# Kernel tuning notes

Measured on AMD Instinct MI355X. Metric: run time of the kernel, lower is better.

Reference implementation:

```python
import jax, jax.numpy as jnp
import numpy as np

BLOCK = 4  # block_size from init_kwargs


def space_to_channel_3d(x, b):
    # Faithful translation of SpaceToChannel_3d.forward (torch split/stack/permute chain).
    B, C, W, H, D = x.shape
    y = x.transpose(0, 2, 3, 4, 1)                      # (B, W, H, D, C)
    y = y.reshape(B, W, H, D // b, b, C)                # split depth into D//b chunks of b
    y = y.transpose(0, 3, 1, 2, 4, 5)                   # (B, D//b, W, H, b, C)
    y = y.reshape(B, D // b, W // b, H // b, C * b * b * b)  # per-chunk row-major reshape
    y = y.transpose(0, 2, 3, 1, 4)                      # (B, W//b, H//b, D//b, C*b^3)
    return y.transpose(0, 4, 1, 2, 3)                   # (B, C*b^3, W//b, H//b, D//b)


def channel_to_space_3d(x, b):
    # Faithful translation of ChannelToSpace_3d.forward.
    B, Cd, wd, hd, dd = x.shape
    b3 = b * b * b
    Cs = Cd // b3
    y = x.transpose(0, 2, 3, 4, 1)                      # (B, wd, hd, dd, Cd)
    y = y.reshape(B, wd, hd, dd, b * b, b, Cs)          # split b^3 dim into b^2 chunks of b
    y = y.transpose(0, 4, 1, 2, 3, 5, 6)                # (B, b^2, wd, hd, dd, b, Cs)
    y = y.reshape(B, b * b, wd, hd, dd * b, Cs)         # merge (dd, b) per chunk
    y = y.transpose(0, 2, 1, 3, 4, 5)                   # (B, wd, b^2, hd, dd*b, Cs)
    y = y.reshape(B, wd * b, hd * b, dd * b, Cs)        # row-major merge of (wd, b^2, hd)
    return y.transpose(0, 4, 1, 2, 3)                   # (B, Cs, wd*b, hd*b, dd*b)


def setup_inputs() -> dict:
    key = jax.random.key(0)
    k1, k2 = jax.random.split(key)
    x = jax.random.normal(k1, (4, 32, 64, 64, 64), dtype=jnp.float32)
    gamma = jax.random.normal(k2, (1,), dtype=jnp.float32)
    return {"x": x, "gamma": gamma}


def reference(x, gamma):
    b = BLOCK
    y = space_to_channel_3d(x, b)                       # (B, C*b^3, w, h, d)
    B, C, w, h, d = y.shape
    q = y.reshape(B, C, w * h * d)                      # (B, C', N)
    # channel-wise attention: energy (B, C', C')
    energy = jnp.einsum('bcn,ben->bce', q, q)
    energy_new = jnp.max(energy, axis=-1, keepdims=True) - energy
    attention = jax.nn.softmax(energy_new, axis=-1)
    out = jnp.einsum('bce,ben->bcn', attention, q)      # (B, C', N)
    out = out.reshape(B, C, w, h, d)
    out = gamma * out + y
    return channel_to_space_3d(out, b)
```

## Files before the change

### kernel.cpp

```cpp
#include <hip/hip_runtime.h>

typedef _Float16 f16;
typedef __attribute__((ext_vector_type(8))) _Float16 f16x8;
typedef __attribute__((ext_vector_type(4))) float f32x4;

#define CCH 2048
#define NSP 4096
#define NB  4

__device__ __forceinline__ void gld16(const void* g, void* l) {
  __builtin_amdgcn_global_load_lds(
      (const __attribute__((address_space(1))) void*)g,
      (__attribute__((address_space(3))) void*)l, 16, 0, 0);
}

__global__ void pack_kernel(const float* __restrict__ x, f16* __restrict__ qh,
                            f16* __restrict__ ql, int b0) {
  int gid = blockIdx.x * 256 + threadIdx.x;
  int n = gid & (NSP - 1);
  int t = gid >> 12;
  int c = t & 31; t >>= 5;
  int r = t & 15; int ib = t >> 4;
  int wc = n >> 8, hc = (n >> 4) & 15, dc = n & 15;
  int w = wc * 4 + (hc >> 2);
  int h = (hc & 3) * 16 + r;
  int b = b0 + ib;
  const f32x4 v = *(const f32x4*)(x + ((((size_t)b * 32 + c) * 64 + w) * 64 + h) * 64 + dc * 4);
#pragma unroll
  for (int bd = 0; bd < 4; ++bd) {
    int cc = r * 128 + bd * 32 + c;
    size_t o = ((size_t)ib * CCH + cc) * NSP + n;
    float val = v[bd];
    f16 hi = (f16)val;
    qh[o] = hi;
    ql[o] = (f16)(val - (float)hi);
  }
}

__global__ void transpose_kernel(const f16* __restrict__ qh, f16* __restrict__ qhT) {
  int ib = blockIdx.z;
  int j0 = blockIdx.x * 64, n0 = blockIdx.y * 64;
  __shared__ f16 tile[64][72];
  int t = threadIdx.x;
  int r = t >> 3;
  int cb = (t & 7) * 8;
#pragma unroll
  for (int half = 0; half < 2; ++half) {
    int rr = r + half * 32;
    f16x8 v = *(const f16x8*)(qh + ((size_t)ib * CCH + j0 + rr) * NSP + n0 + cb);
    *(f16x8*)&tile[rr][cb] = v;
  }
  __syncthreads();
#pragma unroll
  for (int half = 0; half < 2; ++half) {
    int rr = r + half * 32;
    f16x8 o;
#pragma unroll
    for (int u = 0; u < 8; ++u) o[u] = tile[cb + u][rr];
    *(f16x8*)(qhT + ((size_t)ib * NSP + n0 + rr) * CCH + j0 + cb) = o;
  }
}

__global__ __launch_bounds__(256) void gemm1_kernel(const f16* __restrict__ qh,
                                                    const f16* __restrict__ ql,
                                                    float* __restrict__ energy,
                                                    int ksplit) {
  int ib = blockIdx.z;
  int nwg = gridDim.x;
  int cpx = nwg >> 3;
  int bx = blockIdx.x;
  int tri = (bx & 7) * cpx + (bx >> 3);
  int ks = 0;
  if (ksplit == 2) { ks = tri >= 136; tri -= ks * 136; }
  int rem = tri, bi = 0, span = 16;
  while (rem >= span) { rem -= span; ++bi; --span; }
  int bj = bi + rem;
  int i0 = bi * 128, j0 = bj * 128;
  int kbeg = ks * 2048;
  int kend = (ksplit == 2) ? kbeg + 2048 : NSP;
  float* eout = energy + ((size_t)(ks * gridDim.z + ib)) * CCH * CCH;

  __shared__ f16 Lds[2][4][128 * 32];
  int tid = threadIdx.x;
  int lane = tid & 63, wv = tid >> 6;
  int l15 = lane & 15, quad = lane >> 4;
  int wr = (wv >> 1) * 64, wcol = (wv & 1) * 64;
  int swz = (l15 >> 1) & 3;
  int kbs = (lane & 3) ^ ((lane >> 3) & 3);

  const f16* srcA = (wv & 1) ? ql : qh;
  int rbase = (wv < 2) ? i0 : j0;
  const f16* gsrc = srcA + ((size_t)ib * CCH + rbase) * NSP
                    + (size_t)(lane >> 2) * NSP + kbs * 8;

  auto stage = [&](int buf, int kk) {
    f16* ld = &Lds[buf][wv][0];
#pragma unroll
    for (int t = 0; t < 8; ++t)
      gld16(gsrc + (size_t)(t * 16) * NSP + kk, ld + t * 512);
  };

  const f32x4 vzero = {0.f, 0.f, 0.f, 0.f};
  f32x4 acc[4][4];
#pragma unroll
  for (int a = 0; a < 4; ++a)
#pragma unroll
    for (int bq = 0; bq < 4; ++bq) acc[a][bq] = vzero;

  int nk = (kend - kbeg) >> 5;
  stage(0, kbeg);
  __syncthreads();
  for (int it = 0; it < nk; ++it) {
    int cur = it & 1;
    if (it + 1 < nk) stage(cur ^ 1, kbeg + ((it + 1) << 5));
    f16x8 ah[4], al[4], bh[4], bl[4];
#pragma unroll
    for (int mt = 0; mt < 4; ++mt) {
      int row = wr + mt * 16 + l15;
      ah[mt] = *(const f16x8*)&Lds[cur][0][row * 32 + ((quad ^ swz) * 8)];
      al[mt] = *(const f16x8*)&Lds[cur][1][row * 32 + ((quad ^ swz) * 8)];
    }
#pragma unroll
    for (int nt = 0; nt < 4; ++nt) {
      int col = wcol + nt * 16 + l15;
      bh[nt] = *(const f16x8*)&Lds[cur][2][col * 32 + ((quad ^ swz) * 8)];
      bl[nt] = *(const f16x8*)&Lds[cur][3][col * 32 + ((quad ^ swz) * 8)];
    }
    __builtin_amdgcn_s_setprio(1);
#pragma unroll
    for (int mt = 0; mt < 4; ++mt)
#pragma unroll
      for (int nt = 0; nt < 4; ++nt) {
        acc[mt][nt] = __builtin_amdgcn_mfma_f32_16x16x32_f16(ah[mt], bh[nt], acc[mt][nt], 0, 0, 0);
        acc[mt][nt] = __builtin_amdgcn_mfma_f32_16x16x32_f16(ah[mt], bl[nt], acc[mt][nt], 0, 0, 0);
        acc[mt][nt] = __builtin_amdgcn_mfma_f32_16x16x32_f16(al[mt], bh[nt], acc[mt][nt], 0, 0, 0);
      }
    __builtin_amdgcn_s_setprio(0);
    __syncthreads();
  }
  bool diag = (bi == bj);
#pragma unroll
  for (int mt = 0; mt < 4; ++mt)
#pragma unroll
    for (int nt = 0; nt < 4; ++nt)
#pragma unroll
      for (int rg = 0; rg < 4; ++rg) {
        int row = i0 + wr + mt * 16 + quad * 4 + rg;
        int col = j0 + wcol + nt * 16 + l15;
        float v = acc[mt][nt][rg];
        eout[(size_t)row * CCH + col] = v;
        if (!diag) eout[(size_t)col * CCH + row] = v;
      }
}

__global__ void softmax_kernel(const float* __restrict__ e0, const float* __restrict__ e1,
                               int two, const float* __restrict__ gamma_p,
                               f16* __restrict__ attn) {
  int i = blockIdx.x, ib = blockIdx.y;
  const float* r0 = e0 + ((size_t)ib * CCH + i) * CCH;
  const float* r1 = e1 + ((size_t)ib * CCH + i) * CCH;
  f16* arow = attn + ((size_t)ib * CCH + i) * CCH;
  int t = threadIdx.x;
  f32x4 v0 = *(const f32x4*)(r0 + t * 8);
  f32x4 v1 = *(const f32x4*)(r0 + t * 8 + 4);
  if (two) {
    f32x4 u0 = *(const f32x4*)(r1 + t * 8);
    f32x4 u1 = *(const f32x4*)(r1 + t * 8 + 4);
#pragma unroll
    for (int u = 0; u < 4; ++u) { v0[u] += u0[u]; v1[u] += u1[u]; }
  }
  float m = v0[0];
#pragma unroll
  for (int u = 1; u < 4; ++u) m = fminf(m, v0[u]);
#pragma unroll
  for (int u = 0; u < 4; ++u) m = fminf(m, v1[u]);
#pragma unroll
  for (int off = 32; off > 0; off >>= 1) m = fminf(m, __shfl_xor(m, off));
  __shared__ float redA[4], redB[4];
  if ((t & 63) == 0) redA[t >> 6] = m;
  __syncthreads();
  m = fminf(fminf(redA[0], redA[1]), fminf(redA[2], redA[3]));
  float e[8], s = 0.f;
#pragma unroll
  for (int u = 0; u < 4; ++u) { e[u] = __expf(m - v0[u]); s += e[u]; }
#pragma unroll
  for (int u = 0; u < 4; ++u) { e[4 + u] = __expf(m - v1[u]); s += e[4 + u]; }
#pragma unroll
  for (int off = 32; off > 0; off >>= 1) s += __shfl_xor(s, off);
  if ((t & 63) == 0) redB[t >> 6] = s;
  __syncthreads();
  s = redB[0] + redB[1] + redB[2] + redB[3];
  float gamma = *gamma_p;
  float ginv = gamma / s;
  int du = i - t * 8;
  f16x8 o;
#pragma unroll
  for (int u = 0; u < 8; ++u) {
    float v = e[u] * ginv;
    if (u == du) v += 1.0f;
    o[u] = (f16)v;
  }
  *(f16x8*)(arow + t * 8) = o;
}

__global__ __launch_bounds__(512) void gemm2_kernel(const f16* __restrict__ attn,
                                                    const f16* __restrict__ qhT,
                                                    float* __restrict__ out, int b0) {
  int ib = blockIdx.z;
  int lin = blockIdx.x + gridDim.x * blockIdx.y;
  int nwg = gridDim.x * gridDim.y;
  int cpx = nwg >> 3;
  int lin2 = (lin & 7) * cpx + (lin >> 3);
  int i0 = (lin2 & 7) * 256;
  int n0 = (lin2 >> 3) * 256;
  __shared__ f16 Lds[2][2][256 * 32];
  int tid = threadIdx.x;
  int lane = tid & 63, wv = tid >> 6;
  int l15 = lane & 15, quad = lane >> 4;
  int wr = (wv >> 2) * 128;
  int wcol = (wv & 3) * 64;
  int swz = (l15 >> 1) & 3;
  int kbs = (lane & 3) ^ ((lane >> 3) & 3);

  int arr = wv >> 2, rsub = wv & 3;
  const f16* gbase = arr ? (qhT + ((size_t)ib * NSP + n0) * CCH)
                         : (attn + ((size_t)ib * CCH + i0) * CCH);
  const f16* gsrc = gbase + (size_t)(rsub * 64 + (lane >> 2)) * CCH + kbs * 8;

  auto stage = [&](int buf, int kk) {
#pragma unroll
    for (int t = 0; t < 4; ++t)
      gld16(gsrc + (size_t)(t * 16) * CCH + kk,
            &Lds[buf][arr][(rsub * 64 + t * 16) * 32]);
  };

  const f32x4 vzero = {0.f, 0.f, 0.f, 0.f};
  f32x4 acc[8][4];
#pragma unroll
  for (int a = 0; a < 8; ++a)
#pragma unroll
    for (int bq = 0; bq < 4; ++bq) acc[a][bq] = vzero;

  const int nk = CCH >> 5;
  stage(0, 0);
  __syncthreads();
  for (int it = 0; it < nk; ++it) {
    int cur = it & 1;
    if (it + 1 < nk) stage(cur ^ 1, (it + 1) << 5);
    f16x8 af[8], bf[4];
#pragma unroll
    for (int mt = 0; mt < 8; ++mt)
      af[mt] = *(const f16x8*)&Lds[cur][0][(wr + mt * 16 + l15) * 32 + ((quad ^ swz) * 8)];
#pragma unroll
    for (int nt = 0; nt < 4; ++nt)
      bf[nt] = *(const f16x8*)&Lds[cur][1][(wcol + nt * 16 + l15) * 32 + ((quad ^ swz) * 8)];
    __builtin_amdgcn_s_setprio(1);
#pragma unroll
    for (int mt = 0; mt < 8; ++mt)
#pragma unroll
      for (int nt = 0; nt < 4; ++nt)
        acc[mt][nt] = __builtin_amdgcn_mfma_f32_16x16x32_f16(af[mt], bf[nt], acc[mt][nt], 0, 0, 0);
    __builtin_amdgcn_s_setprio(0);
    __syncthreads();
  }

  float* eld = (float*)&Lds[0][0][0];
  int b = b0 + ib;
#pragma unroll
  for (int p = 0; p < 4; ++p) {
    __syncthreads();
    if ((wv >> 1) == p) {
#pragma unroll
      for (int mt = 0; mt < 8; ++mt) {
        int f = mt >> 1;
        int gb2 = (mt & 1) * 16 + quad * 4;
#pragma unroll
        for (int nt = 0; nt < 4; ++nt) {
          int jh = (wv & 1) * 4 + nt;
#pragma unroll
          for (int rg = 0; rg < 4; ++rg)
            eld[(gb2 + rg) * 512 + jh * 64 + l15 * 4 + f] = acc[mt][nt][rg];
        }
      }
    }
    __syncthreads();
    int h = p >> 1, nh = p & 1;
    int e = (i0 >> 7) + h;
    int W = (n0 >> 8) * 4 + (e >> 2);
    int H0 = (e & 3) * 16 + nh * 8;
#pragma unroll
    for (int u = 0; u < 4; ++u) {
      int g = wv * 4 + u;
      size_t goff = ((((size_t)b * 32 + g) * 64 + W) * 4096) + (size_t)H0 * 64;
#pragma unroll
      for (int hv = 0; hv < 2; ++hv) {
        int fo = hv * 256 + lane * 4;
        *(f32x4*)(out + goff + fo) = *(const f32x4*)&eld[g * 512 + fo];
      }
    }
  }
}

extern "C" void kernel_launch(void* const* d_in, const int* in_sizes, int n_in,
                              void* d_out, int out_size, void* d_ws, size_t ws_size,
                              hipStream_t stream) {
  const float* x = (const float*)d_in[0];
  const float* gamma = (const float*)d_in[1];
  float* out = (float*)d_out;

  const size_t szQ = (size_t)CCH * NSP;
  const size_t szE = (size_t)CCH * CCH;

  const size_t pbSplit = szQ * 2 * 3 + szE * 4 * 2 + szE * 2;
  const size_t pbNoSplit = szQ * 2 * 3 + szE * 4 + szE * 2;

  int ksplit, nb;
  if (ws_size >= (size_t)NB * pbSplit) { ksplit = 2; nb = NB; }
  else if (ws_size >= (size_t)NB * pbNoSplit) { ksplit = 1; nb = NB; }
  else { ksplit = 1; nb = 1; }

  char* p = (char*)d_ws;
  f16* qh = (f16*)p;   p += (size_t)nb * szQ * 2;
  f16* ql = (f16*)p;   p += (size_t)nb * szQ * 2;
  f16* qhT = (f16*)p;  p += (size_t)nb * szQ * 2;
  float* energy = (float*)p; p += (size_t)nb * szE * 4 * ksplit;
  f16* attn = (f16*)p;
  const float* e1 = (ksplit == 2) ? (energy + (size_t)nb * szE) : energy;

  for (int b0 = 0; b0 < NB; b0 += nb) {
    pack_kernel<<<nb * 8192, 256, 0, stream>>>(x, qh, ql, b0);
    transpose_kernel<<<dim3(32, 64, nb), 256, 0, stream>>>(qh, qhT);
    gemm1_kernel<<<dim3(136 * ksplit, 1, nb), 256, 0, stream>>>(qh, ql, energy, ksplit);
    softmax_kernel<<<dim3(CCH, nb), 256, 0, stream>>>(energy, e1, ksplit - 1, gamma, attn);
    gemm2_kernel<<<dim3(8, 16, nb), 512, 0, stream>>>(attn, qhT, out, b0);
  }
}
```

Baseline: 689.2 us.

## Restructure gemm2 main loop into 8-phase pipeline with 64-wide K tiles

Rewrites the gemm2 K-loop to use 128KB of dynamic LDS holding double-buffered 256x64 A and B tiles. Each K tile is split into four phases that interleave LDS fragment reads, asynchronous global-to-LDS loads for the next tile, and MFMA work, separated by raw s_barriers and explicit vmcnt waits. A new XOR swizzle is applied over 8 k-chunks. The goal is finer overlap of loads with compute and fewer loop iterations per K, at the cost of more barriers and one workgroup per CU because of the LDS footprint.

```diff
diff --git a/kernel.cpp b/kernel.cpp
--- a/kernel.cpp
+++ b/kernel.cpp
@@ -7,6 +7,8 @@
 #define CCH 2048
 #define NSP 4096
 #define NB  4
+
+#define CFENCE asm volatile("" ::: "memory")
 
 __device__ __forceinline__ void gld16(const void* g, void* l) {
   __builtin_amdgcn_global_load_lds(
@@ -203,9 +205,41 @@
   *(f16x8*)(arow + t * 8) = o;
 }
 
+#define G2_PHASE(D, DN, MTH, KS, SKT, SMAT, SHALF, CK) do {                         \
+    const int k8p = ((KS)*4 + quad) ^ (l15 & 7);                                    \
+    f16x8 af[4], bf[4];                                                             \
+    _Pragma("unroll")                                                               \
+    for (int m2 = 0; m2 < 4; ++m2)                                                  \
+      af[m2] = *(const f16x8*)&lds[(((D)*2 + 0)*2 + hA)*8192 +                      \
+                                   ((MTH)*64 + m2*16 + l15)*64 + k8p*8];            \
+    _Pragma("unroll")                                                               \
+    for (int n2 = 0; n2 < 4; ++n2)                                                  \
+      bf[n2] = *(const f16x8*)&lds[(((D)*2 + 1)*2 + hB)*8192 +                      \
+                                   (bofs + n2*16 + l15)*64 + k8p*8];                \
+    if ((SKT) < 32) {                                                               \
+      const f16* s_ = ((SMAT) ? bsrc : asrc)                                        \
+                      + (size_t)((SHALF)*128 + srow0)*CCH + (SKT)*64 + k8s*8;       \
+      f16* d_ = lds + (((DN)*2 + (SMAT))*2 + (SHALF))*8192 + srow0*64 + k8d*8;      \
+      gld16(s_, d_);                                                                \
+      gld16(s_ + (size_t)64*CCH, d_ + 4096);                                        \
+    }                                                                               \
+    CFENCE; __builtin_amdgcn_s_barrier(); CFENCE;                                   \
+    __builtin_amdgcn_s_setprio(1);                                                  \
+    _Pragma("unroll")                                                               \
+    for (int m2 = 0; m2 < 4; ++m2)                                                  \
+      _Pragma("unroll")                                                             \
+      for (int n2 = 0; n2 < 4; ++n2)                                                \
+        acc[(MTH)*4 + m2][n2] = __builtin_amdgcn_mfma_f32_16x16x32_f16(             \
+            af[m2], bf[n2], acc[(MTH)*4 + m2][n2], 0, 0, 0);                        \
+    __builtin_amdgcn_s_setprio(0);                                                  \
+    if (CK) { asm volatile("s_waitcnt vmcnt(0)" ::: "memory"); }                    \
+    CFENCE; __builtin_amdgcn_s_barrier(); CFENCE;                                   \
+  } while (0)
+
 __global__ __launch_bounds__(512) void gemm2_kernel(const f16* __restrict__ attn,
                                                     const f16* __restrict__ qhT,
                                                     float* __restrict__ out, int b0) {
+  extern __shared__ f16 lds[];
   int ib = blockIdx.z;
   int lin = blockIdx.x + gridDim.x * blockIdx.y;
   int nwg = gridDim.x * gridDim.y;
@@ -213,26 +247,19 @@
   int lin2 = (lin & 7) * cpx + (lin >> 3);
   int i0 = (lin2 & 7) * 256;
   int n0 = (lin2 >> 3) * 256;
-  __shared__ f16 Lds[2][2][256 * 32];
+
   int tid = threadIdx.x;
   int lane = tid & 63, wv = tid >> 6;
   int l15 = lane & 15, quad = lane >> 4;
-  int wr = (wv >> 2) * 128;
-  int wcol = (wv & 3) * 64;
-  int swz = (l15 >> 1) & 3;
-  int kbs = (lane & 3) ^ ((lane >> 3) & 3);
-
-  int arr = wv >> 2, rsub = wv & 3;
-  const f16* gbase = arr ? (qhT + ((size_t)ib * NSP + n0) * CCH)
-                         : (attn + ((size_t)ib * CCH + i0) * CCH);
-  const f16* gsrc = gbase + (size_t)(rsub * 64 + (lane >> 2)) * CCH + kbs * 8;
-
-  auto stage = [&](int buf, int kk) {
-#pragma unroll
-    for (int t = 0; t < 4; ++t)
-      gld16(gsrc + (size_t)(t * 16) * CCH + kk,
-            &Lds[buf][arr][(rsub * 64 + t * 16) * 32]);
-  };
+  const int hA = wv >> 2;
+  const int hB = (wv & 3) >> 1;
+  const int bofs = (wv & 1) * 64;
+  const int srow0 = tid >> 3;
+  const int k8s = (tid & 7) ^ (srow0 & 7);
+  const int k8d = tid & 7;
+
+  const f16* asrc = attn + ((size_t)ib * CCH + i0) * CCH;
+  const f16* bsrc = qhT + ((size_t)ib * NSP + n0) * CCH;
 
   const f32x4 vzero = {0.f, 0.f, 0.f, 0.f};
   f32x4 acc[8][4];
@@ -241,30 +268,34 @@
 #pragma unroll
     for (int bq = 0; bq < 4; ++bq) acc[a][bq] = vzero;
 
-  const int nk = CCH >> 5;
-  stage(0, 0);
-  __syncthreads();
-  for (int it = 0; it < nk; ++it) {
-    int cur = it & 1;
-    if (it + 1 < nk) stage(cur ^ 1, (it + 1) << 5);
-    f16x8 af[8], bf[4];
-#pragma unroll
-    for (int mt = 0; mt < 8; ++mt)
-      af[mt] = *(const f16x8*)&Lds[cur][0][(wr + mt * 16 + l15) * 32 + ((quad ^ swz) * 8)];
-#pragma unroll
-    for (int nt = 0; nt < 4; ++nt)
-      bf[nt] = *(const f16x8*)&Lds[cur][1][(wcol + nt * 16 + l15) * 32 + ((quad ^ swz) * 8)];
-    __builtin_amdgcn_s_setprio(1);
-#pragma unroll
-    for (int mt = 0; mt < 8; ++mt)
-#pragma unroll
-      for (int nt = 0; nt < 4; ++nt)
-        acc[mt][nt] = __builtin_amdgcn_mfma_f32_16x16x32_f16(af[mt], bf[nt], acc[mt][nt], 0, 0, 0);
-    __builtin_amdgcn_s_setprio(0);
-    __syncthreads();
-  }
-
-  float* eld = (float*)&Lds[0][0][0];
+  {
+#pragma unroll
+    for (int sm = 0; sm < 2; ++sm)
+#pragma unroll
+      for (int sh = 0; sh < 2; ++sh) {
+        const f16* s_ = (sm ? bsrc : asrc) + (size_t)(sh * 128 + srow0) * CCH + k8s * 8;
+        f16* d_ = lds + ((0 * 2 + sm) * 2 + sh) * 8192 + srow0 * 64 + k8d * 8;
+        gld16(s_, d_);
+        gld16(s_ + (size_t)64 * CCH, d_ + 4096);
+      }
+    asm volatile("s_waitcnt vmcnt(0)" ::: "memory");
+    CFENCE; __builtin_amdgcn_s_barrier(); CFENCE;
+  }
+
+  for (int it = 0; it < 16; ++it) {
+    int t1 = 2 * it + 1, t2 = 2 * it + 2;
+    G2_PHASE(0, 1, 0, 0, t1, 0, 0, 0);
+    G2_PHASE(0, 1, 1, 0, t1, 1, 0, 0);
+    G2_PHASE(0, 1, 0, 1, t1, 0, 1, 0);
+    G2_PHASE(0, 1, 1, 1, t1, 1, 1, 1);
+    G2_PHASE(1, 0, 0, 0, t2, 0, 0, 0);
+    G2_PHASE(1, 0, 1, 0, t2, 1, 0, 0);
+    G2_PHASE(1, 0, 0, 1, t2, 0, 1, 0);
+    G2_PHASE(1, 0, 1, 1, t2, 1, 1, 1);
+  }
+
+  __syncthreads();
+  float* eld = (float*)lds;
   int b = b0 + ib;
 #pragma unroll
   for (int p = 0; p < 4; ++p) {
@@ -307,6 +338,13 @@
   const float* x = (const float*)d_in[0];
   const float* gamma = (const float*)d_in[1];
   float* out = (float*)d_out;
+
+  static bool g2cfg = false;
+  if (!g2cfg) {
+    hipFuncSetAttribute(reinterpret_cast<const void*>(gemm2_kernel),
+                        hipFuncAttributeMaxDynamicSharedMemorySize, 131072);
+    g2cfg = true;
+  }
 
   const size_t szQ = (size_t)CCH * NSP;
   const size_t szE = (size_t)CCH * CCH;
@@ -332,6 +370,6 @@
     transpose_kernel<<<dim3(32, 64, nb), 256, 0, stream>>>(qh, qhT);
     gemm1_kernel<<<dim3(136 * ksplit, 1, nb), 256, 0, stream>>>(qh, ql, energy, ksplit);
     softmax_kernel<<<dim3(CCH, nb), 256, 0, stream>>>(energy, e1, ksplit - 1, gamma, attn);
-    gemm2_kernel<<<dim3(8, 16, nb), 512, 0, stream>>>(attn, qhT, out, b0);
-  }
-}
+    gemm2_kernel<<<dim3(8, 16, nb), 512, 131072, stream>>>(attn, qhT, out, b0);
+  }
+}
```

After: 682.3 us. No clear change (-1.0%).
